# Kernel optimization log

Measured on AMD Instinct MI355X. Metric: run time of the kernel, lower is better.

## Reference

```python
import jax, jax.numpy as jnp
import numpy as np

DT = 0.1  # integration step used by LiquidCell.forward default

def setup_inputs() -> dict:
    key = jax.random.key(0)
    k1, k2, k3 = jax.random.split(key, 3)
    B, T, I, H = 32, 1024, 512, 1024
    x = jax.random.normal(k1, (B, T, I), dtype=jnp.float32)
    # Linear weights stored torch-style: [out_features, in_features]
    W = jax.random.normal(k2, (H, I), dtype=jnp.float32) * 0.02
    U = jax.random.normal(k3, (H, H), dtype=jnp.float32) * 0.02
    b = jnp.zeros((H,), dtype=jnp.float32)
    tau = jnp.ones((H,), dtype=jnp.float32)
    return {"x": x, "W": W, "U": U, "b": b, "tau": tau}

def reference(x, W, U, b, tau):
    # x: [B, T, I]; returns (h_final [B, H], all_states [B, T, H])
    B = x.shape[0]
    H = tau.shape[0]
    # Precompute input projections for all timesteps in one big GEMM: [B, T, H]
    xW = jnp.einsum('bti,hi->bth', x, W)
    inv_tau = 1.0 / tau

    def step(h, xW_t):
        # xW_t: [B, H]
        act = jnp.tanh(xW_t + h @ U.T + b)
        h_new = h + DT * (-inv_tau * h + act)
        return h_new, h_new

    h0 = jnp.zeros((B, H), dtype=x.dtype)
    xs = jnp.swapaxes(xW, 0, 1)  # [T, B, H]
    h_final, states = jax.lax.scan(step, h0, xs)
    all_states = jnp.swapaxes(states, 0, 1)  # [B, T, H]
    return h_final, all_states
```

## Files before the change

kernel.cpp:

```cpp
#include <hip/hip_runtime.h>


#define DT 0.1f
#define BB 32
#define TT 1024
#define II 512
#define HH 1024

typedef __attribute__((ext_vector_type(4))) float f32x4;
typedef __attribute__((ext_vector_type(8))) short s16x8;

__device__ __forceinline__ unsigned short f2bf(float f) {
  unsigned int u = __builtin_bit_cast(unsigned int, f);
  u += 0x7fffu + ((u >> 16) & 1u);
  return (unsigned short)(u >> 16);
}

__global__ __launch_bounds__(256) void cvt_u_kernel(const float* __restrict__ U,
                                                    unsigned short* __restrict__ Ub) {
  int i4 = (blockIdx.x * 256 + threadIdx.x) * 4;
  float4 v = *(const float4*)(U + i4);
  ushort4 o;
  o.x = f2bf(v.x); o.y = f2bf(v.y); o.z = f2bf(v.z); o.w = f2bf(v.w);
  *(ushort4*)(Ub + i4) = o;
}

#define P1_LDK 36

__global__ __launch_bounds__(256) void xw_gemm(const float* __restrict__ x,
                                               const float* __restrict__ W,
                                               float* __restrict__ out) {
  __shared__ __align__(16) float Xs[128 * P1_LDK];
  __shared__ __align__(16) float Ws_s[128 * P1_LDK];
  const int tid = threadIdx.x;
  const int m0 = blockIdx.y * 128;
  const int n0 = blockIdx.x * 128;
  const int ty = tid >> 4;
  const int tx = tid & 15;
  const int lrow = tid >> 3;
  const int lf = tid & 7;

  float acc[8][8];
#pragma unroll
  for (int i = 0; i < 8; ++i)
#pragma unroll
    for (int j = 0; j < 8; ++j) acc[i][j] = 0.0f;

  for (int kk = 0; kk < II; kk += 32) {
#pragma unroll
    for (int p = 0; p < 4; ++p) {
      int r = lrow + 32 * p;
      float4 vx = *(const float4*)&x[(m0 + r) * II + kk + 4 * lf];
      *(float4*)&Xs[r * P1_LDK + 4 * lf] = vx;
      float4 vw = *(const float4*)&W[(n0 + r) * II + kk + 4 * lf];
      *(float4*)&Ws_s[r * P1_LDK + 4 * lf] = vw;
    }
    __syncthreads();
#pragma unroll
    for (int kq = 0; kq < 32; kq += 4) {
      float4 a[8], b[8];
#pragma unroll
      for (int i = 0; i < 4; ++i) {
        a[i]     = *(const float4*)&Xs[(ty * 4 + i) * P1_LDK + kq];
        a[i + 4] = *(const float4*)&Xs[(ty * 4 + i + 64) * P1_LDK + kq];
      }
#pragma unroll
      for (int j = 0; j < 8; ++j)
        b[j] = *(const float4*)&Ws_s[(tx + 16 * j) * P1_LDK + kq];
#pragma unroll
      for (int i = 0; i < 8; ++i)
#pragma unroll
        for (int j = 0; j < 8; ++j) {
          acc[i][j] += a[i].x * b[j].x;
          acc[i][j] += a[i].y * b[j].y;
          acc[i][j] += a[i].z * b[j].z;
          acc[i][j] += a[i].w * b[j].w;
        }
    }
    __syncthreads();
  }
#pragma unroll
  for (int i = 0; i < 8; ++i) {
    int m = m0 + ty * 4 + (i < 4 ? i : 64 + i - 4);
#pragma unroll
    for (int j = 0; j < 8; ++j)
      out[m * HH + n0 + tx + 16 * j] = acc[i][j];
  }
}

#define LDH 1032

__global__ __launch_bounds__(64) void liquid_step(
    const unsigned short* __restrict__ hb,
    const unsigned short* __restrict__ Ub,
    float* __restrict__ hf,
    unsigned short* __restrict__ hb_out,
    float* __restrict__ states,
    const float* __restrict__ bias,
    const float* __restrict__ tau,
    int t) {
  __shared__ __align__(16) unsigned short h_s[16 * LDH];
  __shared__ __align__(16) unsigned short u_s[8 * LDH];

  const int l = threadIdx.x;
  const int bid = blockIdx.x;
  const int mg = bid >> 7;
  const int jg = bid & 127;
  const int n = l & 15;
  const int q = l >> 4;
  const int jloc = n & 7;
  const int j = jg * 8 + jloc;

  float xw[4], hold[4];
#pragma unroll
  for (int r = 0; r < 4; ++r) {
    int b = mg * 16 + q * 4 + r;
    xw[r] = states[(b * TT + t) * HH + j];
    hold[r] = hf[b * HH + j];
  }
  float bj = bias[j];
  float invt = 1.0f / tau[j];

#pragma unroll
  for (int r = 0; r < 16; ++r) {
    int b = mg * 16 + r;
#pragma unroll
    for (int hh = 0; hh < 2; ++hh) {
      uint4 v = *(const uint4*)(hb + b * HH + hh * 512 + l * 8);
      *(uint4*)&h_s[r * LDH + hh * 512 + l * 8] = v;
    }
  }
#pragma unroll
  for (int r = 0; r < 8; ++r) {
    int jr = jg * 8 + r;
#pragma unroll
    for (int hh = 0; hh < 2; ++hh) {
      uint4 v = *(const uint4*)(Ub + jr * HH + hh * 512 + l * 8);
      *(uint4*)&u_s[r * LDH + hh * 512 + l * 8] = v;
    }
  }
  __syncthreads();

  f32x4 acc0 = {0.f, 0.f, 0.f, 0.f}, acc1 = {0.f, 0.f, 0.f, 0.f};
  const int ar = n;
  const int br = jloc;
  const int ko = q * 8;
#pragma unroll
  for (int kc = 0; kc < 32; kc += 2) {
    s16x8 a0 = *(const s16x8*)&h_s[ar * LDH + kc * 32 + ko];
    s16x8 b0 = *(const s16x8*)&u_s[br * LDH + kc * 32 + ko];
    acc0 = __builtin_amdgcn_mfma_f32_16x16x32_bf16(a0, b0, acc0, 0, 0, 0);
    s16x8 a1 = *(const s16x8*)&h_s[ar * LDH + (kc + 1) * 32 + ko];
    s16x8 b1 = *(const s16x8*)&u_s[br * LDH + (kc + 1) * 32 + ko];
    acc1 = __builtin_amdgcn_mfma_f32_16x16x32_bf16(a1, b1, acc1, 0, 0, 0);
  }
  f32x4 acc = acc0 + acc1;

#pragma unroll
  for (int r = 0; r < 4; ++r) {
    float pre = xw[r] + acc[r] + bj;
    float act = tanhf(pre);
    float hnew = hold[r] + DT * (act - invt * hold[r]);
    if (n < 8) {
      int b = mg * 16 + q * 4 + r;
      hf[b * HH + j] = hnew;
      hb_out[b * HH + j] = f2bf(hnew);
      states[(b * TT + t) * HH + j] = hnew;
    }
  }
}

extern "C" void kernel_launch(void* const* d_in, const int* in_sizes, int n_in,
                              void* d_out, int out_size, void* d_ws, size_t ws_size,
                              hipStream_t stream) {
  const float* x    = (const float*)d_in[0];
  const float* W    = (const float*)d_in[1];
  const float* U    = (const float*)d_in[2];
  const float* bias = (const float*)d_in[3];
  const float* tau  = (const float*)d_in[4];

  float* out = (float*)d_out;
  float* hf = out;
  float* states = out + BB * HH;

  unsigned short* Ub = (unsigned short*)d_ws;
  unsigned short* hb = Ub + (size_t)HH * HH;

  hipMemsetAsync(hf, 0, BB * HH * sizeof(float), stream);
  hipMemsetAsync(hb, 0, BB * HH * sizeof(unsigned short), stream);

  cvt_u_kernel<<<(HH * HH) / (256 * 4), 256, 0, stream>>>(U, Ub);

  xw_gemm<<<dim3(HH / 128, (BB * TT) / 128), 256, 0, stream>>>(x, W, states);

  for (int t = 0; t < TT; ++t) {
    liquid_step<<<256, 64, 0, stream>>>(hb, Ub, hf, hb, states, bias, tau, t);
  }
}
```

Baseline: 5.045 ms.

## Replace per-timestep launches with persistent scan kernel using grid barrier

Replaces the 1024 per-timestep kernel launches with one persistent kernel of 32 workgroups that loops over all timesteps and synchronizes through per-step atomic counters in global memory. Each workgroup keeps its slice of U in registers as bf16 MFMA fragments, so the separate conversion kernel and the per-step reload of U are gone. The hidden state is double-buffered in global memory and staged into LDS with async global-to-LDS loads and a swizzled layout. This removes launch overhead and repeated weight traffic. In exchange it relies on all 32 workgroups being co-resident for the spin barrier, and the split-K reduction now goes through LDS.

```diff
diff --git a/kernel.cpp b/kernel.cpp
--- a/kernel.cpp
+++ b/kernel.cpp
@@ -6,6 +6,7 @@
 #define TT 1024
 #define II 512
 #define HH 1024
+#define NWG 32
 
 typedef __attribute__((ext_vector_type(4))) float f32x4;
 typedef __attribute__((ext_vector_type(8))) short s16x8;
@@ -16,13 +17,10 @@
   return (unsigned short)(u >> 16);
 }
 
-__global__ __launch_bounds__(256) void cvt_u_kernel(const float* __restrict__ U,
-                                                    unsigned short* __restrict__ Ub) {
-  int i4 = (blockIdx.x * 256 + threadIdx.x) * 4;
-  float4 v = *(const float4*)(U + i4);
-  ushort4 o;
-  o.x = f2bf(v.x); o.y = f2bf(v.y); o.z = f2bf(v.z); o.w = f2bf(v.w);
-  *(ushort4*)(Ub + i4) = o;
+__device__ __forceinline__ void async16(const void* g, void* l) {
+  __builtin_amdgcn_global_load_lds(
+      (const __attribute__((address_space(1))) unsigned int*)g,
+      (__attribute__((address_space(3))) unsigned int*)l, 16, 0, 0);
 }
 
 #define P1_LDK 36
@@ -88,84 +86,145 @@
   }
 }
 
-#define LDH 1032
-
-__global__ __launch_bounds__(64) void liquid_step(
-    const unsigned short* __restrict__ hb,
-    const unsigned short* __restrict__ Ub,
-    float* __restrict__ hf,
-    unsigned short* __restrict__ hb_out,
-    float* __restrict__ states,
-    const float* __restrict__ bias,
-    const float* __restrict__ tau,
-    int t) {
-  __shared__ __align__(16) unsigned short h_s[16 * LDH];
-  __shared__ __align__(16) unsigned short u_s[8 * LDH];
-
-  const int l = threadIdx.x;
-  const int bid = blockIdx.x;
-  const int mg = bid >> 7;
-  const int jg = bid & 127;
+__global__ __launch_bounds__(256, 1) void liquid_scan(
+    const float* __restrict__ U, const float* __restrict__ bias,
+    const float* __restrict__ tau, float* __restrict__ hf,
+    float* __restrict__ states, unsigned short* __restrict__ hb0,
+    unsigned short* __restrict__ hb1, int* __restrict__ ctr) {
+  __shared__ __align__(16) unsigned short h_s[BB * HH];
+  __shared__ float red[2][2][4][64];
+
+  const int tid = threadIdx.x;
+  const int l = tid & 63;
+  const int wv = tid >> 6;
+  const int mt = wv & 1;
+  const int kh = wv >> 1;
   const int n = l & 15;
   const int q = l >> 4;
-  const int jloc = n & 7;
-  const int j = jg * 8 + jloc;
-
-  float xw[4], hold[4];
-#pragma unroll
-  for (int r = 0; r < 4; ++r) {
-    int b = mg * 16 + q * 4 + r;
-    xw[r] = states[(b * TT + t) * HH + j];
-    hold[r] = hf[b * HH + j];
-  }
-  float bj = bias[j];
-  float invt = 1.0f / tau[j];
-
-#pragma unroll
-  for (int r = 0; r < 16; ++r) {
-    int b = mg * 16 + r;
-#pragma unroll
-    for (int hh = 0; hh < 2; ++hh) {
-      uint4 v = *(const uint4*)(hb + b * HH + hh * 512 + l * 8);
-      *(uint4*)&h_s[r * LDH + hh * 512 + l * 8] = v;
-    }
-  }
-#pragma unroll
-  for (int r = 0; r < 8; ++r) {
-    int jr = jg * 8 + r;
-#pragma unroll
-    for (int hh = 0; hh < 2; ++hh) {
-      uint4 v = *(const uint4*)(Ub + jr * HH + hh * 512 + l * 8);
-      *(uint4*)&u_s[r * LDH + hh * 512 + l * 8] = v;
-    }
-  }
-  __syncthreads();
-
-  f32x4 acc0 = {0.f, 0.f, 0.f, 0.f}, acc1 = {0.f, 0.f, 0.f, 0.f};
-  const int ar = n;
-  const int br = jloc;
-  const int ko = q * 8;
-#pragma unroll
-  for (int kc = 0; kc < 32; kc += 2) {
-    s16x8 a0 = *(const s16x8*)&h_s[ar * LDH + kc * 32 + ko];
-    s16x8 b0 = *(const s16x8*)&u_s[br * LDH + kc * 32 + ko];
-    acc0 = __builtin_amdgcn_mfma_f32_16x16x32_bf16(a0, b0, acc0, 0, 0, 0);
-    s16x8 a1 = *(const s16x8*)&h_s[ar * LDH + (kc + 1) * 32 + ko];
-    s16x8 b1 = *(const s16x8*)&u_s[br * LDH + (kc + 1) * 32 + ko];
-    acc1 = __builtin_amdgcn_mfma_f32_16x16x32_bf16(a1, b1, acc1, 0, 0, 0);
-  }
-  f32x4 acc = acc0 + acc1;
-
-#pragma unroll
-  for (int r = 0; r < 4; ++r) {
-    float pre = xw[r] + acc[r] + bj;
-    float act = tanhf(pre);
-    float hnew = hold[r] + DT * (act - invt * hold[r]);
-    if (n < 8) {
-      int b = mg * 16 + q * 4 + r;
-      hf[b * HH + j] = hnew;
-      hb_out[b * HH + j] = f2bf(hnew);
-      states[(b * TT + t) * HH + j] = hnew;
+  const int j0 = blockIdx.x * 32;
+
+  s16x8 Bfrag[2][16];
+#pragma unroll
+  for (int jt = 0; jt < 2; ++jt) {
+    int j = j0 + jt * 16 + n;
+#pragma unroll
+    for (int ks = 0; ks < 16; ++ks) {
+      int kb = kh * 512 + ks * 32 + q * 8;
+      float4 u0 = *(const float4*)&U[j * HH + kb];
+      float4 u1 = *(const float4*)&U[j * HH + kb + 4];
+      s16x8 bf;
+      bf[0] = (short)f2bf(u0.x); bf[1] = (short)f2bf(u0.y);
+      bf[2] = (short)f2bf(u0.z); bf[3] = (short)f2bf(u0.w);
+      bf[4] = (short)f2bf(u1.x); bf[5] = (short)f2bf(u1.y);
+      bf[6] = (short)f2bf(u1.z); bf[7] = (short)f2bf(u1.w);
+      Bfrag[jt][ks] = bf;
+    }
+  }
+
+  int aaddr[16];
+  const int r_a = mt * 16 + n;
+#pragma unroll
+  for (int ks = 0; ks < 16; ++ks) {
+    int kc = (kh * 16 + ks) * 4 + q;
+    aaddr[ks] = (r_a * 128 + (kc ^ (r_a & 7))) * 16;
+  }
+
+  int goff[16];
+#pragma unroll
+  for (int p = 0; p < 16; ++p) {
+    int C = (wv * 16 + p) * 64 + l;
+    int b = C >> 7;
+    int kc = (C & 127) ^ (b & 7);
+    goff[p] = b * 2048 + kc * 16;
+  }
+
+  float invt[2], bj[2];
+  long long xwoff[2][4];
+  float h_own[2][4];
+  float xwv[2][4];
+  if (kh == 0) {
+#pragma unroll
+    for (int jt = 0; jt < 2; ++jt) {
+      int j = j0 + jt * 16 + n;
+      bj[jt] = bias[j];
+      invt[jt] = 1.0f / tau[j];
+#pragma unroll
+      for (int rr = 0; rr < 4; ++rr) {
+        int b = mt * 16 + q * 4 + rr;
+        xwoff[jt][rr] = ((long long)b * TT * HH + j) * 4;
+        h_own[jt][rr] = 0.0f;
+        xwv[jt][rr] = *(const float*)((const char*)states + xwoff[jt][rr]);
+      }
+    }
+  }
+
+#pragma unroll 1
+  for (int t = 0; t < TT; ++t) {
+    const unsigned short* hcur = (t & 1) ? hb1 : hb0;
+    unsigned short* hnxt = (t & 1) ? hb0 : hb1;
+
+#pragma unroll
+    for (int p = 0; p < 16; ++p)
+      async16((const char*)hcur + goff[p], (char*)h_s + (wv * 16 + p) * 1024);
+    __syncthreads();
+
+    f32x4 acc0 = {0.f, 0.f, 0.f, 0.f}, acc1 = {0.f, 0.f, 0.f, 0.f};
+#pragma unroll
+    for (int ks = 0; ks < 16; ++ks) {
+      s16x8 a = *(const s16x8*)((const char*)h_s + aaddr[ks]);
+      acc0 = __builtin_amdgcn_mfma_f32_16x16x32_bf16(a, Bfrag[0][ks], acc0, 0, 0, 0);
+      acc1 = __builtin_amdgcn_mfma_f32_16x16x32_bf16(a, Bfrag[1][ks], acc1, 0, 0, 0);
+    }
+
+    if (kh == 1) {
+#pragma unroll
+      for (int rr = 0; rr < 4; ++rr) {
+        red[mt][0][rr][l] = acc0[rr];
+        red[mt][1][rr][l] = acc1[rr];
+      }
+    }
+    __syncthreads();
+
+    if (kh == 0) {
+#pragma unroll
+      for (int jt = 0; jt < 2; ++jt) {
+#pragma unroll
+        for (int rr = 0; rr < 4; ++rr) {
+          float dot = (jt ? acc1[rr] : acc0[rr]) + red[mt][jt][rr][l];
+          float pre = xwv[jt][rr] + dot + bj[jt];
+          float act = tanhf(pre);
+          float h = h_own[jt][rr];
+          float hnew = h + DT * (act - invt[jt] * h);
+          h_own[jt][rr] = hnew;
+          int b = mt * 16 + q * 4 + rr;
+          int j = j0 + jt * 16 + n;
+          *(float*)((char*)states + xwoff[jt][rr] + (long long)t * (HH * 4)) = hnew;
+          hnxt[b * HH + j] = f2bf(hnew);
+          if (t == TT - 1) hf[b * HH + j] = hnew;
+        }
+      }
+      if (t + 1 < TT) {
+#pragma unroll
+        for (int jt = 0; jt < 2; ++jt)
+#pragma unroll
+          for (int rr = 0; rr < 4; ++rr)
+            xwv[jt][rr] = *(const float*)((const char*)states + xwoff[jt][rr] +
+                                          (long long)(t + 1) * (HH * 4));
+      }
+    }
+
+    if (t < TT - 1) {
+      __threadfence();
+      __syncthreads();
+      if (tid == 0) {
+        __hip_atomic_fetch_add(&ctr[t], 1, __ATOMIC_RELEASE,
+                               __HIP_MEMORY_SCOPE_AGENT);
+        while (__hip_atomic_load(&ctr[t], __ATOMIC_ACQUIRE,
+                                 __HIP_MEMORY_SCOPE_AGENT) < NWG)
+          __builtin_amdgcn_s_sleep(1);
+      }
+      __syncthreads();
+      __threadfence();
     }
   }
 }
@@ -183,17 +242,13 @@
   float* hf = out;
   float* states = out + BB * HH;
 
-  unsigned short* Ub = (unsigned short*)d_ws;
-  unsigned short* hb = Ub + (size_t)HH * HH;
-
-  hipMemsetAsync(hf, 0, BB * HH * sizeof(float), stream);
-  hipMemsetAsync(hb, 0, BB * HH * sizeof(unsigned short), stream);
-
-  cvt_u_kernel<<<(HH * HH) / (256 * 4), 256, 0, stream>>>(U, Ub);
+  unsigned short* hb0 = (unsigned short*)d_ws;
+  unsigned short* hb1 = hb0 + BB * HH;
+  int* ctr = (int*)((char*)d_ws + 2 * BB * HH * 2);
+
+  hipMemsetAsync(hb0, 0, BB * HH * 2, stream);
+  hipMemsetAsync(ctr, 0, TT * 4, stream);
 
   xw_gemm<<<dim3(HH / 128, (BB * TT) / 128), 256, 0, stream>>>(x, W, states);
-
-  for (int t = 0; t < TT; ++t) {
-    liquid_step<<<256, 64, 0, stream>>>(hb, Ub, hf, hb, states, bias, tau, t);
-  }
-}
+  liquid_scan<<<NWG, 256, 0, stream>>>(U, bias, tau, hf, states, hb0, hb1, ctr);
+}
```

Measured after the change: 8.807 ms. 1.75x slower.
